# Performance work log

Measured on AMD Instinct MI355X. Metric: run time of the kernel, lower is better.

Reference implementation:

```python
import jax, jax.numpy as jnp
import numpy as np

H = 1024
LENGTH = 48
N = 2048


def setup_inputs() -> dict:
    key = jax.random.key(0)
    k1, k2, k3, k4 = jax.random.split(key, 4)
    s = 1.0 / np.sqrt(H)  # torch LSTMCell init: U(-1/sqrt(H), 1/sqrt(H))
    h_in = jax.random.normal(k1, (N, H), dtype=jnp.float32)
    W_hh = jax.random.uniform(k2, (4 * H, H), minval=-s, maxval=s, dtype=jnp.float32)
    b_ih = jax.random.uniform(k3, (4 * H,), minval=-s, maxval=s, dtype=jnp.float32)
    b_hh = jax.random.uniform(k4, (4 * H,), minval=-s, maxval=s, dtype=jnp.float32)
    return {"h_in": h_in, "W_hh": W_hh, "b_ih": b_ih, "b_hh": b_hh}


def reference(h_in, W_hh, b_ih, b_hh):
    # LSTMCell with input_size=0: gates depend only on hidden state.
    # torch gate order: i, f, g, o.
    Hd = h_in.shape[1]
    bias = b_ih + b_hh
    c0 = jnp.zeros_like(h_in)

    def step(carry, _):
        h, c = carry
        z = h @ W_hh.T + bias  # (N, 4H)
        i = jax.nn.sigmoid(z[:, :Hd])
        f = jax.nn.sigmoid(z[:, Hd:2 * Hd])
        g = jnp.tanh(z[:, 2 * Hd:3 * Hd])
        o = jax.nn.sigmoid(z[:, 3 * Hd:])
        c_new = f * c + i * g
        h_new = o * jnp.tanh(c_new)
        return (h_new, c_new), h_new

    _, hs = jax.lax.scan(step, (h_in, c0), None, length=LENGTH)  # (L, N, H)
    return jnp.transpose(hs, (1, 2, 0))  # (N, H, L) matching torch.stack(axis=-1)
```

## Files before the change

### kernel.cpp

```cpp
#include <hip/hip_runtime.h>
#include <hip/hip_bf16.h>

#define Hdim 1024
#define Nb   2048
#define Lsteps 48

#define BM 256
#define BROWS 128
#define NT 16
#define DEPTH 3

typedef unsigned short ushort_t;
typedef short bf16x8 __attribute__((ext_vector_type(8)));
typedef float f32x4 __attribute__((ext_vector_type(4)));

typedef __attribute__((address_space(3))) unsigned int lds_u32;
typedef const __attribute__((address_space(1))) unsigned int glb_u32;

__device__ __forceinline__ void gll16(const void* g, void* l) {
    __builtin_amdgcn_global_load_lds((glb_u32*)g, (lds_u32*)l, 16, 0, 0);
}

__device__ __forceinline__ ushort_t f2bf(float x) {
    unsigned u = __builtin_bit_cast(unsigned, x);
    unsigned r = u + 0x7fffu + ((u >> 16) & 1u);
    return (ushort_t)(r >> 16);
}

__device__ __forceinline__ float frcp(float x) { return __builtin_amdgcn_rcpf(x); }
__device__ __forceinline__ float fsigmoid(float x) { return frcp(1.0f + __expf(-x)); }
__device__ __forceinline__ float ftanh(float x) {
    float xm = fminf(fmaxf(x, -15.0f), 15.0f);
    float e = __expf(2.0f * xm);
    return (e - 1.0f) * frcp(e + 1.0f);
}

__device__ __forceinline__ f32x4 mfma16(bf16x8 a, bf16x8 b, f32x4 c) {
    return __builtin_amdgcn_mfma_f32_16x16x32_bf16(a, b, c, 0, 0, 0);
}

#define VMCNT12  asm volatile("s_waitcnt vmcnt(12)" ::: "memory")
#define VMCNT6   asm volatile("s_waitcnt vmcnt(6)"  ::: "memory")
#define VMCNT0   asm volatile("s_waitcnt vmcnt(0)"  ::: "memory")
#define LGKMCNT0 asm volatile("s_waitcnt lgkmcnt(0)" ::: "memory")

__global__ __launch_bounds__(256) void prep_w(const float* __restrict__ W,
                                              ushort_t* __restrict__ Wb) {
    int i = blockIdx.x * 256 + threadIdx.x;
    Wb[i] = f2bf(W[i]);
}

__global__ __launch_bounds__(256) void prep_h(const float* __restrict__ h_in,
                                              ushort_t* __restrict__ h0,
                                              const float* __restrict__ b_ih,
                                              const float* __restrict__ b_hh,
                                              float* __restrict__ bias) {
    int i = blockIdx.x * 256 + threadIdx.x;
    h0[i] = f2bf(h_in[i]);
    if (i < 4 * Hdim) bias[i] = b_ih[i] + b_hh[i];
}

__global__ __launch_bounds__(512, 2) void lstm_step(
    const ushort_t* __restrict__ hsrc,
    ushort_t* __restrict__ hdst,
    const ushort_t* __restrict__ Wb,
    const float* __restrict__ bias,
    float* __restrict__ cst,
    float* __restrict__ tmp)
{
    extern __shared__ __align__(16) ushort_t smem[];
    ushort_t* As = smem;
    ushort_t* Bs = smem + DEPTH * (BM * 64);

    const int tid  = threadIdx.x;
    const int lane = tid & 63;
    const int wid  = tid >> 6;
    const int wr   = wid >> 1;
    const int wc   = wid & 1;

    const int p    = blockIdx.x;
    const int xcd  = p & 7;
    const int slot = p >> 3;
    const int jb   = (xcd >> 1) * 8 + (slot & 7);
    const int nb   = (xcd & 1) * 4 + (slot >> 3);
    const int n0   = nb * BM;
    const int j0   = jb * 32;

    const int lr   = lane & 15;
    const int q4   = (lane >> 4) * 4;
    const int j    = j0 + wc * 16 + lr;

    float cpre[16];
#pragma unroll
    for (int ri = 0; ri < 4; ++ri)
#pragma unroll
        for (int q = 0; q < 4; ++q)
            cpre[ri * 4 + q] = cst[(size_t)(n0 + wr * 64 + ri * 16 + q4 + q) * Hdim + j];
    const float bi = bias[j];
    const float bf = bias[Hdim + j];
    const float bg = bias[2 * Hdim + j];
    const float bo = bias[3 * Hdim + j];

    f32x4 acc[4][4];
#pragma unroll
    for (int g = 0; g < 4; ++g)
#pragma unroll
        for (int ri = 0; ri < 4; ++ri)
            acc[g][ri] = (f32x4){0.f, 0.f, 0.f, 0.f};

    const int srow8  = lane >> 3;
    const int schunk = (lane & 7) ^ srow8;
    const int choff  = schunk * 8;

    const ushort_t* aGlob = hsrc + (size_t)(n0 + wid * 32 + srow8) * Hdim + choff;
    const ushort_t* bGlob = Wb + (size_t)((wid >> 1) * Hdim + j0 + (wid & 1) * 16 + srow8) * Hdim + choff;

    const int rsw  = lr & 7;
    const int cq   = lane >> 4;

    auto STAGE = [&](int buf, int it) {
        const int k0 = it * 64;
#pragma unroll
        for (int ii = 0; ii < 4; ++ii)
            gll16(aGlob + (size_t)ii * 8 * Hdim + k0,
                  &As[buf * (BM * 64) + (wid * 32 + ii * 8) * 64]);
#pragma unroll
        for (int ii = 0; ii < 2; ++ii)
            gll16(bGlob + (size_t)ii * 8 * Hdim + k0,
                  &Bs[buf * (BROWS * 64) + (wid * 16 + ii * 8) * 64]);
    };

    auto COMPUTE = [&](int buf) {
#pragma unroll
        for (int kh = 0; kh < 2; ++kh) {
            const int ch = ((cq + kh * 4) ^ rsw) * 8;
            bf16x8 af[4], bfr[4];
#pragma unroll
            for (int ri = 0; ri < 4; ++ri) {
                int row = wr * 64 + ri * 16 + lr;
                af[ri] = *(const bf16x8*)&As[buf * (BM * 64) + row * 64 + ch];
            }
#pragma unroll
            for (int g = 0; g < 4; ++g) {
                int u = g * 32 + wc * 16 + lr;
                bfr[g] = *(const bf16x8*)&Bs[buf * (BROWS * 64) + u * 64 + ch];
            }
#pragma unroll
            for (int g = 0; g < 4; ++g)
#pragma unroll
                for (int ri = 0; ri < 4; ++ri)
                    acc[g][ri] = mfma16(af[ri], bfr[g], acc[g][ri]);
        }
    };

    STAGE(0, 0); STAGE(1, 1); STAGE(2, 2);
    int cur = 0;
#pragma unroll 1
    for (int t = 0; t < NT; ++t) {
        if (t <= NT - 3)      { VMCNT12; }
        else if (t == NT - 2) { VMCNT6;  }
        else                  { VMCNT0;  }
        __builtin_amdgcn_s_barrier();
        __builtin_amdgcn_s_setprio(1);
        COMPUTE(cur);
        __builtin_amdgcn_s_setprio(0);
        if (t <= NT - 4) {
            LGKMCNT0;
            __builtin_amdgcn_s_barrier();
            STAGE(cur, t + 3);
        }
        cur = (cur == 2) ? 0 : cur + 1;
    }

#pragma unroll
    for (int ri = 0; ri < 4; ++ri)
#pragma unroll
        for (int q = 0; q < 4; ++q) {
            int n = n0 + wr * 64 + ri * 16 + q4 + q;
            float gi = fsigmoid(acc[0][ri][q] + bi);
            float gf = fsigmoid(acc[1][ri][q] + bf);
            float gg = ftanh(acc[2][ri][q] + bg);
            float go = fsigmoid(acc[3][ri][q] + bo);
            size_t idx = (size_t)n * Hdim + j;
            float cn = gf * cpre[ri * 4 + q] + gi * gg;
            cst[idx] = cn;
            float hv = go * ftanh(cn);
            hdst[idx] = f2bf(hv);
            tmp[idx] = hv;
        }
}

__global__ __launch_bounds__(256) void flush16(const float* __restrict__ tmp,
                                               float* __restrict__ out, int t0) {
    int idx = blockIdx.x * 256 + threadIdx.x;
    float v[16];
#pragma unroll
    for (int s = 0; s < 16; ++s)
        v[s] = tmp[(size_t)s * (Nb * Hdim) + idx];
    float4* dst = (float4*)(out + (size_t)idx * Lsteps + t0);
#pragma unroll
    for (int s = 0; s < 4; ++s)
        dst[s] = make_float4(v[4 * s], v[4 * s + 1], v[4 * s + 2], v[4 * s + 3]);
}

extern "C" void kernel_launch(void* const* d_in, const int* in_sizes, int n_in,
                              void* d_out, int out_size, void* d_ws, size_t ws_size,
                              hipStream_t stream) {
    const float* h_in = (const float*)d_in[0];
    const float* W    = (const float*)d_in[1];
    const float* b_ih = (const float*)d_in[2];
    const float* b_hh = (const float*)d_in[3];
    float* out = (float*)d_out;

    char* ws = (char*)d_ws;
    ushort_t* Wb   = (ushort_t*)(ws);
    ushort_t* h0   = (ushort_t*)(ws + 8388608);
    ushort_t* h1   = (ushort_t*)(ws + 12582912);
    float*    cst  = (float*)(ws + 16777216);
    float*    bias = (float*)(ws + 25165824);
    float*    tmp16= (float*)(ws + 25182208);

    static bool attr_done = false;
    if (!attr_done) {
        hipFuncSetAttribute((const void*)lstm_step,
                            hipFuncAttributeMaxDynamicSharedMemorySize,
                            DEPTH * (BM * 64 + BROWS * 64) * (int)sizeof(ushort_t));
        attr_done = true;
    }
    const int smem_bytes = DEPTH * (BM * 64 + BROWS * 64) * (int)sizeof(ushort_t);

    hipMemsetAsync(cst, 0, (size_t)Nb * Hdim * sizeof(float), stream);

    prep_w<<<(4 * Hdim * Hdim) / 256, 256, 0, stream>>>(W, Wb);
    prep_h<<<(Nb * Hdim) / 256, 256, 0, stream>>>(h_in, h0, b_ih, b_hh, bias);

    for (int t = 0; t < Lsteps; ++t) {
        const ushort_t* hs = (t & 1) ? h1 : h0;
        ushort_t*       hd = (t & 1) ? h0 : h1;
        float* tslot = tmp16 + (size_t)(t & 15) * (Nb * Hdim);
        lstm_step<<<256, 512, smem_bytes, stream>>>(hs, hd, Wb, bias, cst, tslot);
        if ((t & 15) == 15) {
            flush16<<<(Nb * Hdim) / 256, 256, 0, stream>>>(tmp16, out, t - 15);
        }
    }
}
```

Measured before the change: 1.784 ms.

## Fuse all LSTM timesteps into one persistent cooperative kernel with grid sync

Result: slower. 5.667 ms (+217.7%).

```diff
diff --git a/kernel.cpp b/kernel.cpp
--- a/kernel.cpp
+++ b/kernel.cpp
@@ -1,5 +1,8 @@
 #include <hip/hip_runtime.h>
 #include <hip/hip_bf16.h>
+#include <hip/hip_cooperative_groups.h>
+
+namespace cg = cooperative_groups;
 
 #define Hdim 1024
 #define Nb   2048
@@ -8,7 +11,6 @@
 #define BM 256
 #define BROWS 128
 #define NT 16
-#define DEPTH 3
 
 typedef unsigned short ushort_t;
 typedef short bf16x8 __attribute__((ext_vector_type(8)));
@@ -39,7 +41,6 @@
     return __builtin_amdgcn_mfma_f32_16x16x32_bf16(a, b, c, 0, 0, 0);
 }
 
-#define VMCNT12  asm volatile("s_waitcnt vmcnt(12)" ::: "memory")
 #define VMCNT6   asm volatile("s_waitcnt vmcnt(6)"  ::: "memory")
 #define VMCNT0   asm volatile("s_waitcnt vmcnt(0)"  ::: "memory")
 #define LGKMCNT0 asm volatile("s_waitcnt lgkmcnt(0)" ::: "memory")
@@ -60,17 +61,19 @@
     if (i < 4 * Hdim) bias[i] = b_ih[i] + b_hh[i];
 }
 
-__global__ __launch_bounds__(512, 2) void lstm_step(
-    const ushort_t* __restrict__ hsrc,
-    ushort_t* __restrict__ hdst,
+__global__ __launch_bounds__(512) void lstm_all(
+    ushort_t* __restrict__ hA,
+    ushort_t* __restrict__ hB,
     const ushort_t* __restrict__ Wb,
     const float* __restrict__ bias,
-    float* __restrict__ cst,
-    float* __restrict__ tmp)
+    float* __restrict__ tmp16,
+    float* __restrict__ out)
 {
     extern __shared__ __align__(16) ushort_t smem[];
     ushort_t* As = smem;
-    ushort_t* Bs = smem + DEPTH * (BM * 64);
+    ushort_t* Bs = smem + 2 * (BM * 64);
+
+    cg::grid_group grid = cg::this_grid();
 
     const int tid  = threadIdx.x;
     const int lane = tid & 63;
@@ -90,117 +93,128 @@
     const int q4   = (lane >> 4) * 4;
     const int j    = j0 + wc * 16 + lr;
 
-    float cpre[16];
-#pragma unroll
-    for (int ri = 0; ri < 4; ++ri)
-#pragma unroll
-        for (int q = 0; q < 4; ++q)
-            cpre[ri * 4 + q] = cst[(size_t)(n0 + wr * 64 + ri * 16 + q4 + q) * Hdim + j];
     const float bi = bias[j];
     const float bf = bias[Hdim + j];
     const float bg = bias[2 * Hdim + j];
     const float bo = bias[3 * Hdim + j];
 
-    f32x4 acc[4][4];
-#pragma unroll
-    for (int g = 0; g < 4; ++g)
-#pragma unroll
-        for (int ri = 0; ri < 4; ++ri)
-            acc[g][ri] = (f32x4){0.f, 0.f, 0.f, 0.f};
+    float cpre[16];
+#pragma unroll
+    for (int i = 0; i < 16; ++i) cpre[i] = 0.0f;
 
     const int srow8  = lane >> 3;
     const int schunk = (lane & 7) ^ srow8;
     const int choff  = schunk * 8;
-
-    const ushort_t* aGlob = hsrc + (size_t)(n0 + wid * 32 + srow8) * Hdim + choff;
-    const ushort_t* bGlob = Wb + (size_t)((wid >> 1) * Hdim + j0 + (wid & 1) * 16 + srow8) * Hdim + choff;
+    const size_t aOff = (size_t)(n0 + wid * 32 + srow8) * Hdim + choff;
+    const ushort_t* bGlob =
+        Wb + (size_t)((wid >> 1) * Hdim + j0 + (wid & 1) * 16 + srow8) * Hdim + choff;
 
     const int rsw  = lr & 7;
     const int cq   = lane >> 4;
 
-    auto STAGE = [&](int buf, int it) {
-        const int k0 = it * 64;
-#pragma unroll
-        for (int ii = 0; ii < 4; ++ii)
-            gll16(aGlob + (size_t)ii * 8 * Hdim + k0,
-                  &As[buf * (BM * 64) + (wid * 32 + ii * 8) * 64]);
-#pragma unroll
-        for (int ii = 0; ii < 2; ++ii)
-            gll16(bGlob + (size_t)ii * 8 * Hdim + k0,
-                  &Bs[buf * (BROWS * 64) + (wid * 16 + ii * 8) * 64]);
-    };
-
-    auto COMPUTE = [&](int buf) {
-#pragma unroll
-        for (int kh = 0; kh < 2; ++kh) {
-            const int ch = ((cq + kh * 4) ^ rsw) * 8;
-            bf16x8 af[4], bfr[4];
-#pragma unroll
-            for (int ri = 0; ri < 4; ++ri) {
-                int row = wr * 64 + ri * 16 + lr;
-                af[ri] = *(const bf16x8*)&As[buf * (BM * 64) + row * 64 + ch];
-            }
-#pragma unroll
-            for (int g = 0; g < 4; ++g) {
-                int u = g * 32 + wc * 16 + lr;
-                bfr[g] = *(const bf16x8*)&Bs[buf * (BROWS * 64) + u * 64 + ch];
-            }
-#pragma unroll
-            for (int g = 0; g < 4; ++g)
-#pragma unroll
-                for (int ri = 0; ri < 4; ++ri)
-                    acc[g][ri] = mfma16(af[ri], bfr[g], acc[g][ri]);
+#pragma unroll 1
+    for (int t = 0; t < Lsteps; ++t) {
+        const ushort_t* hsrc = (t & 1) ? hB : hA;
+        ushort_t*       hdst = (t & 1) ? hA : hB;
+        float* tslot = tmp16 + (size_t)(t & 15) * (Nb * Hdim);
+        const ushort_t* aGlob = hsrc + aOff;
+
+        f32x4 acc[4][4];
+#pragma unroll
+        for (int g = 0; g < 4; ++g)
+#pragma unroll
+            for (int ri = 0; ri < 4; ++ri)
+                acc[g][ri] = (f32x4){0.f, 0.f, 0.f, 0.f};
+
+        auto STAGE = [&](int buf, int it) {
+            const int k0 = it * 64;
+#pragma unroll
+            for (int ii = 0; ii < 4; ++ii)
+                gll16(aGlob + (size_t)ii * 8 * Hdim + k0,
+                      &As[buf * (BM * 64) + (wid * 32 + ii * 8) * 64]);
+#pragma unroll
+            for (int ii = 0; ii < 2; ++ii)
+                gll16(bGlob + (size_t)ii * 8 * Hdim + k0,
+                      &Bs[buf * (BROWS * 64) + (wid * 16 + ii * 8) * 64]);
+        };
+
+        auto COMPUTE = [&](int buf) {
+#pragma unroll
+            for (int kh = 0; kh < 2; ++kh) {
+                const int ch = ((cq + kh * 4) ^ rsw) * 8;
+                bf16x8 af[4], bfr[4];
+#pragma unroll
+                for (int ri = 0; ri < 4; ++ri) {
+                    int row = wr * 64 + ri * 16 + lr;
+                    af[ri] = *(const bf16x8*)&As[buf * (BM * 64) + row * 64 + ch];
+                }
+#pragma unroll
+                for (int g = 0; g < 4; ++g) {
+                    int u = g * 32 + wc * 16 + lr;
+                    bfr[g] = *(const bf16x8*)&Bs[buf * (BROWS * 64) + u * 64 + ch];
+                }
+#pragma unroll
+                for (int g = 0; g < 4; ++g)
+#pragma unroll
+                    for (int ri = 0; ri < 4; ++ri)
+                        acc[g][ri] = mfma16(af[ri], bfr[g], acc[g][ri]);
+            }
+        };
+
+        STAGE(0, 0); STAGE(1, 1);
+#pragma unroll 1
+        for (int tt = 0; tt < NT; ++tt) {
+            const int cur = tt & 1;
+            if (tt < NT - 1) { VMCNT6; } else { VMCNT0; }
+            __builtin_amdgcn_s_barrier();
+            __builtin_amdgcn_s_setprio(1);
+            COMPUTE(cur);
+            __builtin_amdgcn_s_setprio(0);
+            if (tt < NT - 2) {
+                LGKMCNT0;
+                __builtin_amdgcn_s_barrier();
+                STAGE(cur, tt + 2);
+            }
         }
-    };
-
-    STAGE(0, 0); STAGE(1, 1); STAGE(2, 2);
-    int cur = 0;
+
+#pragma unroll
+        for (int ri = 0; ri < 4; ++ri)
+#pragma unroll
+            for (int q = 0; q < 4; ++q) {
+                int n = n0 + wr * 64 + ri * 16 + q4 + q;
+                float gi = fsigmoid(acc[0][ri][q] + bi);
+                float gf = fsigmoid(acc[1][ri][q] + bf);
+                float gg = ftanh(acc[2][ri][q] + bg);
+                float go = fsigmoid(acc[3][ri][q] + bo);
+                size_t idx = (size_t)n * Hdim + j;
+                float cn = gf * cpre[ri * 4 + q] + gi * gg;
+                cpre[ri * 4 + q] = cn;
+                float hv = go * ftanh(cn);
+                hdst[idx] = f2bf(hv);
+                tslot[idx] = hv;
+            }
+
+        __threadfence();
+        grid.sync();
+
+        if ((t & 15) == 15) {
+            const int t0 = t - 15;
+            const int gth = blockIdx.x * 512 + tid;
 #pragma unroll 1
-    for (int t = 0; t < NT; ++t) {
-        if (t <= NT - 3)      { VMCNT12; }
-        else if (t == NT - 2) { VMCNT6;  }
-        else                  { VMCNT0;  }
-        __builtin_amdgcn_s_barrier();
-        __builtin_amdgcn_s_setprio(1);
-        COMPUTE(cur);
-        __builtin_amdgcn_s_setprio(0);
-        if (t <= NT - 4) {
-            LGKMCNT0;
-            __builtin_amdgcn_s_barrier();
-            STAGE(cur, t + 3);
+            for (int u = 0; u < 16; ++u) {
+                int idx = u * 131072 + gth;
+                float v[16];
+#pragma unroll
+                for (int s = 0; s < 16; ++s)
+                    v[s] = tmp16[(size_t)s * (Nb * Hdim) + idx];
+                float4* dst = (float4*)(out + (size_t)idx * Lsteps + t0);
+#pragma unroll
+                for (int s = 0; s < 4; ++s)
+                    dst[s] = make_float4(v[4 * s], v[4 * s + 1], v[4 * s + 2], v[4 * s + 3]);
+            }
+            grid.sync();
         }
-        cur = (cur == 2) ? 0 : cur + 1;
     }
-
-#pragma unroll
-    for (int ri = 0; ri < 4; ++ri)
-#pragma unroll
-        for (int q = 0; q < 4; ++q) {
-            int n = n0 + wr * 64 + ri * 16 + q4 + q;
-            float gi = fsigmoid(acc[0][ri][q] + bi);
-            float gf = fsigmoid(acc[1][ri][q] + bf);
-            float gg = ftanh(acc[2][ri][q] + bg);
-            float go = fsigmoid(acc[3][ri][q] + bo);
-            size_t idx = (size_t)n * Hdim + j;
-            float cn = gf * cpre[ri * 4 + q] + gi * gg;
-            cst[idx] = cn;
-            float hv = go * ftanh(cn);
-            hdst[idx] = f2bf(hv);
-            tmp[idx] = hv;
-        }
-}
-
-__global__ __launch_bounds__(256) void flush16(const float* __restrict__ tmp,
-                                               float* __restrict__ out, int t0) {
-    int idx = blockIdx.x * 256 + threadIdx.x;
-    float v[16];
-#pragma unroll
-    for (int s = 0; s < 16; ++s)
-        v[s] = tmp[(size_t)s * (Nb * Hdim) + idx];
-    float4* dst = (float4*)(out + (size_t)idx * Lsteps + t0);
-#pragma unroll
-    for (int s = 0; s < 4; ++s)
-        dst[s] = make_float4(v[4 * s], v[4 * s + 1], v[4 * s + 2], v[4 * s + 3]);
 }
 
 extern "C" void kernel_launch(void* const* d_in, const int* in_sizes, int n_in,
@@ -216,31 +230,22 @@
     ushort_t* Wb   = (ushort_t*)(ws);
     ushort_t* h0   = (ushort_t*)(ws + 8388608);
     ushort_t* h1   = (ushort_t*)(ws + 12582912);
-    float*    cst  = (float*)(ws + 16777216);
-    float*    bias = (float*)(ws + 25165824);
-    float*    tmp16= (float*)(ws + 25182208);
-
+    float*    bias = (float*)(ws + 16777216);
+    float*    tmp16= (float*)(ws + 16793600);
+
+    const int smem_bytes = 2 * (BM * 64 + BROWS * 64) * (int)sizeof(ushort_t);
     static bool attr_done = false;
     if (!attr_done) {
-        hipFuncSetAttribute((const void*)lstm_step,
-                            hipFuncAttributeMaxDynamicSharedMemorySize,
-                            DEPTH * (BM * 64 + BROWS * 64) * (int)sizeof(ushort_t));
+        hipFuncSetAttribute((const void*)lstm_all,
+                            hipFuncAttributeMaxDynamicSharedMemorySize, smem_bytes);
         attr_done = true;
     }
-    const int smem_bytes = DEPTH * (BM * 64 + BROWS * 64) * (int)sizeof(ushort_t);
-
-    hipMemsetAsync(cst, 0, (size_t)Nb * Hdim * sizeof(float), stream);
 
     prep_w<<<(4 * Hdim * Hdim) / 256, 256, 0, stream>>>(W, Wb);
     prep_h<<<(Nb * Hdim) / 256, 256, 0, stream>>>(h_in, h0, b_ih, b_hh, bias);
 
-    for (int t = 0; t < Lsteps; ++t) {
-        const ushort_t* hs = (t & 1) ? h1 : h0;
-        ushort_t*       hd = (t & 1) ? h0 : h1;
-        float* tslot = tmp16 + (size_t)(t & 15) * (Nb * Hdim);
-        lstm_step<<<256, 512, smem_bytes, stream>>>(hs, hd, Wb, bias, cst, tslot);
-        if ((t & 15) == 15) {
-            flush16<<<(Nb * Hdim) / 256, 256, 0, stream>>>(tmp16, out, t - 15);
-        }
-    }
-}
+    void* kargs[] = { (void*)&h0, (void*)&h1, (void*)&Wb, (void*)&bias,
+                      (void*)&tmp16, (void*)&out };
+    hipLaunchCooperativeKernel((const void*)lstm_all, dim3(256), dim3(512),
+                               kargs, smem_bytes, stream);
+}
```
